# Kernel optimization log

Hardware: AMD Instinct MI355X
Metric: run time of the kernel (lower is better)

## Reference

```python
import jax, jax.numpy as jnp
import numpy as np

B, S, D_IN, D_EMB = 8, 2048, 512, 512

def setup_inputs() -> dict:
    key = jax.random.key(0)
    ks = jax.random.split(key, 7)
    s = 1.0 / np.sqrt(D_IN)
    return {
        "x": jax.random.normal(ks[0], (B, S, D_IN), dtype=jnp.float32),
        "Wq": jax.random.uniform(ks[1], (D_IN, D_EMB), jnp.float32, -s, s),
        "bq": jax.random.uniform(ks[2], (D_EMB,), jnp.float32, -s, s),
        "Wk": jax.random.uniform(ks[3], (D_IN, D_EMB), jnp.float32, -s, s),
        "bk": jax.random.uniform(ks[4], (D_EMB,), jnp.float32, -s, s),
        "Wv": jax.random.uniform(ks[5], (D_IN, D_EMB), jnp.float32, -s, s),
        "bv": jax.random.uniform(ks[6], (D_EMB,), jnp.float32, -s, s),
    }

def reference(x, Wq, bq, Wk, bk, Wv, bv):
    # single-head attention: softmax(QK^T / sqrt(d)) V
    q = x @ Wq + bq            # [B,S,E]
    k = x @ Wk + bk
    v = x @ Wv + bv
    scores = jnp.einsum('bse,bte->bst', q, k) / jnp.sqrt(jnp.float32(D_EMB))
    attn = jax.nn.softmax(scores, axis=-1)  # [B,S,S]
    return jnp.einsum('bst,bte->bse', attn, v)
```

## Files before the change

kernel.cpp:

```cpp
#include <hip/hip_runtime.h>
#include <stdint.h>


using f32x4 = __attribute__((ext_vector_type(4))) float;
using s16x8 = __attribute__((ext_vector_type(8))) short;
using u16x4 = __attribute__((ext_vector_type(4))) unsigned short;

#define S_LEN 2048
#define EMB   512

#define ASYNC16(g, l)                                                     \
  __builtin_amdgcn_global_load_lds(                                       \
      (const __attribute__((address_space(1))) void*)(g),                 \
      (__attribute__((address_space(3))) void*)(l), 16, 0, 0)

__device__ __forceinline__ unsigned short f2bf(float f) {
  union { float f; unsigned u; } v; v.f = f;
  unsigned r = v.u + 0x7fffu + ((v.u >> 16) & 1u);
  return (unsigned short)(r >> 16);
}

__global__ __launch_bounds__(256) void xconv_kernel(
    const float* __restrict__ x, short* __restrict__ xb) {
  int i = (blockIdx.x * 256 + threadIdx.x) * 8;
  f32x4 a = *(const f32x4*)(x + i);
  f32x4 b = *(const f32x4*)(x + i + 4);
  s16x8 h;
  h[0] = (short)f2bf(a[0]); h[1] = (short)f2bf(a[1]);
  h[2] = (short)f2bf(a[2]); h[3] = (short)f2bf(a[3]);
  h[4] = (short)f2bf(b[0]); h[5] = (short)f2bf(b[1]);
  h[6] = (short)f2bf(b[2]); h[7] = (short)f2bf(b[3]);
  *(s16x8*)(xb + i) = h;
}

__global__ __launch_bounds__(256) void wconv_kernel(
    const float* __restrict__ Wq, const float* __restrict__ Wk,
    const float* __restrict__ Wv, short* __restrict__ Wt) {
  int idx = blockIdx.x * 256 + threadIdx.x;
  int mat = idx >> 18;
  int r   = idx & 262143;
  int n   = r >> 9;
  int k   = r & 511;
  const float* W = (mat == 0) ? Wq : (mat == 1) ? Wk : Wv;
  Wt[idx] = (short)f2bf(W[k * 512 + n]);
}

__global__ __launch_bounds__(256) void qkv_gemm(
    const short* __restrict__ xb, const short* __restrict__ Wt,
    const float* __restrict__ bq, const float* __restrict__ bk,
    const float* __restrict__ bv,
    short* __restrict__ Qg, short* __restrict__ Kg, short* __restrict__ VTg) {
  __shared__ __align__(16) short As[128 * 64];
  __shared__ __align__(16) short Bs[128 * 64];
  int gid = blockIdx.x;
  int mat = gid >> 9;
  int rem = gid & 511;
  int mt  = rem & 127, nt = rem >> 7;
  int m0  = mt << 7,   n0 = nt << 7;
  const short* W    = Wt + (size_t)mat * 262144;
  const float* bias = (mat == 0) ? bq : (mat == 1) ? bk : bv;

  int tid = threadIdx.x, lane = tid & 63, wv = tid >> 6;
  int l16 = lane & 15, quad = lane >> 4;
  int wr = (wv & 1) << 6, wc = (wv >> 1) << 6;
  int drow = lane >> 3;
  int dchk = (lane & 7) ^ drow;

  const f32x4 Z4 = {0.f, 0.f, 0.f, 0.f};
  f32x4 acc[4][4];
#pragma unroll
  for (int a = 0; a < 4; ++a)
#pragma unroll
    for (int c = 0; c < 4; ++c) acc[a][c] = Z4;

  for (int it = 0; it < 8; ++it) {
    int k0 = it << 6;
    __syncthreads();
#pragma unroll
    for (int i = 0; i < 4; ++i) {
      int g   = wv * 4 + i;
      int row = g * 8 + drow;
      ASYNC16(xb + (size_t)(m0 + row) * 512 + k0 + dchk * 8, &As[g * 512]);
    }
#pragma unroll
    for (int i = 0; i < 4; ++i) {
      int g   = wv * 4 + i;
      int row = g * 8 + drow;
      ASYNC16(W + (size_t)(n0 + row) * 512 + k0 + dchk * 8, &Bs[g * 512]);
    }
    __syncthreads();
#pragma unroll
    for (int kk = 0; kk < 2; ++kk) {
      s16x8 af[4], bfr[4];
#pragma unroll
      for (int rb = 0; rb < 4; ++rb) {
        int row = wr + rb * 16 + l16;
        int c   = kk * 4 + quad;
        af[rb] = *(const s16x8*)(As + row * 64 + ((c ^ (row & 7)) * 8));
      }
#pragma unroll
      for (int cb = 0; cb < 4; ++cb) {
        int row = wc + cb * 16 + l16;
        int c   = kk * 4 + quad;
        bfr[cb] = *(const s16x8*)(Bs + row * 64 + ((c ^ (row & 7)) * 8));
      }
#pragma unroll
      for (int rb = 0; rb < 4; ++rb)
#pragma unroll
        for (int cb = 0; cb < 4; ++cb)
          acc[rb][cb] = __builtin_amdgcn_mfma_f32_16x16x32_bf16(af[rb], bfr[cb], acc[rb][cb], 0, 0, 0);
    }
  }

  float bsv[4];
#pragma unroll
  for (int cb = 0; cb < 4; ++cb) bsv[cb] = bias[n0 + wc + cb * 16 + l16];

  if (mat < 2) {
    short* D = (mat == 0) ? Qg : Kg;
#pragma unroll
    for (int rb = 0; rb < 4; ++rb)
#pragma unroll
      for (int cb = 0; cb < 4; ++cb)
#pragma unroll
        for (int r = 0; r < 4; ++r) {
          int m = m0 + wr + rb * 16 + quad * 4 + r;
          D[(size_t)m * 512 + n0 + wc + cb * 16 + l16] =
              (short)f2bf(acc[rb][cb][r] + bsv[cb]);
        }
  } else {
#pragma unroll
    for (int rb = 0; rb < 4; ++rb)
#pragma unroll
      for (int cb = 0; cb < 4; ++cb) {
        u16x4 h;
#pragma unroll
        for (int r = 0; r < 4; ++r) h[r] = f2bf(acc[rb][cb][r] + bsv[cb]);
        int m  = m0 + wr + rb * 16 + quad * 4;
        int bb = m >> 11, s = m & 2047;
        int e  = n0 + wc + cb * 16 + l16;
        *(u16x4*)(VTg + ((size_t)bb * 512 + e) * 2048 + s) = h;
      }
  }
}

__global__ __launch_bounds__(256, 2) void attn_kernel(
    const short* __restrict__ Qg, const short* __restrict__ Kg,
    const short* __restrict__ VTg, float* __restrict__ out) {
  __shared__ __align__(16) short Kt[32 * 512];
  __shared__ __align__(16) short Vt[512 * 32];
  __shared__ __align__(16) short Pl[32 * 48];
  __shared__ float l_l[32];
  const float SCL2 = 0.06375871855f;

  int b = blockIdx.x & 7, qt = blockIdx.x >> 3;
  int s0 = qt << 5;
  int tid = threadIdx.x, lane = tid & 63, wv = tid >> 6;
  int l16 = lane & 15, quad = lane >> 4;
  int a = wv & 1, h = wv >> 1;
  int e0 = wv << 7;

  const short* Kb = Kg  + ((size_t)b * S_LEN) * 512;
  const short* Vb = VTg + ((size_t)b * 512) * 2048;

  const short* kdma[8];
#pragma unroll
  for (int i = 0; i < 8; ++i) {
    int r = wv * 8 + i;
    kdma[i] = Kb + (size_t)r * 512 + ((lane ^ (i & 7)) * 8);
  }
  int v_er = lane >> 2;
  const short* vdma[8];
#pragma unroll
  for (int i = 0; i < 8; ++i) {
    int g = wv * 8 + i;
    int e = g * 16 + v_er;
    int vc = (lane & 3) ^ ((e >> 1) & 3);
    vdma[i] = Vb + (size_t)e * 2048 + vc * 8;
  }

#pragma unroll
  for (int i = 0; i < 8; ++i)
    ASYNC16(kdma[i], &Kt[(wv * 8 + i) * 512]);

  const short* qrow = Qg + ((size_t)b * S_LEN + s0 + a * 16 + l16) * 512 + quad * 8;
  s16x8 qf[16];
#pragma unroll
  for (int kk = 0; kk < 16; ++kk) qf[kk] = *(const s16x8*)(qrow + kk * 32);

  const f32x4 Z4 = {0.f, 0.f, 0.f, 0.f};
  f32x4 acc[2][8];
#pragma unroll
  for (int rb = 0; rb < 2; ++rb)
#pragma unroll
    for (int cb = 0; cb < 8; ++cb) acc[rb][cb] = Z4;
  f32x4 lsum = Z4;

  __syncthreads();

  for (int kt = 0; kt < 64; ++kt) {
    int t0 = kt << 5;
#pragma unroll
    for (int i = 0; i < 8; ++i)
      ASYNC16(vdma[i] + t0, &Vt[(wv * 8 + i) * 512]);

    f32x4 s_a = Z4, s_b = Z4;
    int krow = h * 16 + l16;
    const short* kb = &Kt[krow * 512];
    int ksw = (krow & 7);
#pragma unroll
    for (int kk = 0; kk < 8; ++kk) {
      s16x8 kf0 = *(const s16x8*)(kb + (((2 * kk) * 4 + quad) ^ ksw) * 8);
      s_a = __builtin_amdgcn_mfma_f32_16x16x32_bf16(qf[2 * kk], kf0, s_a, 0, 0, 0);
      s16x8 kf1 = *(const s16x8*)(kb + (((2 * kk + 1) * 4 + quad) ^ ksw) * 8);
      s_b = __builtin_amdgcn_mfma_f32_16x16x32_bf16(qf[2 * kk + 1], kf1, s_b, 0, 0, 0);
    }
    f32x4 sv = s_a + s_b;

    unsigned short pb[4];
#pragma unroll
    for (int r = 0; r < 4; ++r) {
      float p = exp2f(sv[r] * SCL2);
      pb[r] = f2bf(p);
      lsum[r] += p;
    }
#pragma unroll
    for (int r = 0; r < 4; ++r)
      Pl[(a * 16 + quad * 4 + r) * 48 + h * 16 + l16] = (short)pb[r];

    __syncthreads();

    if (kt + 1 < 64) {
      size_t adv = (size_t)(kt + 1) * 32 * 512;
#pragma unroll
      for (int i = 0; i < 8; ++i)
        ASYNC16(kdma[i] + adv, &Kt[(wv * 8 + i) * 512]);
    }

    s16x8 pf[2];
#pragma unroll
    for (int rb = 0; rb < 2; ++rb)
      pf[rb] = *(const s16x8*)(Pl + (rb * 16 + l16) * 48 + quad * 8);
#pragma unroll
    for (int cb = 0; cb < 8; ++cb) {
      int e  = e0 + cb * 16 + l16;
      int pc = quad ^ ((e >> 1) & 3);
      s16x8 vf = *(const s16x8*)(Vt + e * 32 + pc * 8);
#pragma unroll
      for (int rb = 0; rb < 2; ++rb)
        acc[rb][cb] = __builtin_amdgcn_mfma_f32_16x16x32_bf16(pf[rb], vf, acc[rb][cb], 0, 0, 0);
    }

    __syncthreads();
  }

#pragma unroll
  for (int r = 0; r < 4; ++r) {
    float v = lsum[r];
    v += __shfl_xor(v, 1);
    v += __shfl_xor(v, 2);
    v += __shfl_xor(v, 4);
    v += __shfl_xor(v, 8);
    lsum[r] = v;
  }
  if (h == 0 && l16 == 0) {
#pragma unroll
    for (int r = 0; r < 4; ++r) l_l[a * 16 + quad * 4 + r] = lsum[r];
  }
  __syncthreads();
  if (h == 1 && l16 == 0) {
#pragma unroll
    for (int r = 0; r < 4; ++r) l_l[a * 16 + quad * 4 + r] += lsum[r];
  }
  __syncthreads();

#pragma unroll
  for (int rb = 0; rb < 2; ++rb) {
    f32x4 lv = *(const f32x4*)(l_l + rb * 16 + quad * 4);
    f32x4 li;
#pragma unroll
    for (int r = 0; r < 4; ++r) li[r] = 1.0f / lv[r];
#pragma unroll
    for (int cb = 0; cb < 8; ++cb)
#pragma unroll
      for (int r = 0; r < 4; ++r)
        out[((size_t)b * S_LEN + s0 + rb * 16 + quad * 4 + r) * 512 + e0 + cb * 16 + l16] =
            acc[rb][cb][r] * li[r];
  }
}

extern "C" void kernel_launch(void* const* d_in, const int* in_sizes, int n_in,
                              void* d_out, int out_size, void* d_ws, size_t ws_size,
                              hipStream_t stream) {
  const float* x  = (const float*)d_in[0];
  const float* Wq = (const float*)d_in[1];
  const float* bq = (const float*)d_in[2];
  const float* Wk = (const float*)d_in[3];
  const float* bk = (const float*)d_in[4];
  const float* Wv = (const float*)d_in[5];
  const float* bv = (const float*)d_in[6];

  short* Wt  = (short*)d_ws;
  short* xb  = (short*)((char*)d_ws + 1572864);
  short* Qg  = xb + (size_t)8388608;
  short* Kg  = Qg + (size_t)8388608;
  short* VTg = Kg + (size_t)8388608;

  xconv_kernel<<<4096, 256, 0, stream>>>(x, xb);
  wconv_kernel<<<3072, 256, 0, stream>>>(Wq, Wk, Wv, Wt);
  qkv_gemm<<<1536, 256, 0, stream>>>(xb, Wt, bq, bk, bv, Qg, Kg, VTg);
  attn_kernel<<<512, 256, 0, stream>>>(Qg, Kg, VTg, (float*)d_out);
}
```

Before: 258.9 us.

## Widen attention key tile to 64, read V from global, share K fragments

The attention loop now handles 64 keys per iteration instead of 32, halving the iteration count and the number of block barriers. Each wave owns 16 keys and computes scores for both 16-row query halves, so one K fragment load from LDS feeds two MFMAs. The V shared-memory tile is removed and V fragments are loaded straight from global memory (L2) inside the PV stage. The trade-offs are a larger K tile in LDS, more registers for two sets of Q fragments, and exposed global-load latency on V with no prefetch, which may hurt occupancy or stall the MFMA pipeline.

```diff
diff --git a/kernel.cpp b/kernel.cpp
--- a/kernel.cpp
+++ b/kernel.cpp
@@ -147,146 +147,134 @@
 __global__ __launch_bounds__(256, 2) void attn_kernel(
     const short* __restrict__ Qg, const short* __restrict__ Kg,
     const short* __restrict__ VTg, float* __restrict__ out) {
-  __shared__ __align__(16) short Kt[32 * 512];
-  __shared__ __align__(16) short Vt[512 * 32];
-  __shared__ __align__(16) short Pl[32 * 48];
-  __shared__ float l_l[32];
+  __shared__ __align__(16) short Kt[64 * 512];
+  __shared__ __align__(16) short Pl[32 * 72];
+  __shared__ float Ls[4][32];
   const float SCL2 = 0.06375871855f;
 
   int b = blockIdx.x & 7, qt = blockIdx.x >> 3;
   int s0 = qt << 5;
   int tid = threadIdx.x, lane = tid & 63, wv = tid >> 6;
   int l16 = lane & 15, quad = lane >> 4;
-  int a = wv & 1, h = wv >> 1;
+  int kq = wv;
   int e0 = wv << 7;
 
   const short* Kb = Kg  + ((size_t)b * S_LEN) * 512;
   const short* Vb = VTg + ((size_t)b * 512) * 2048;
 
-  const short* kdma[8];
-#pragma unroll
-  for (int i = 0; i < 8; ++i) {
-    int r = wv * 8 + i;
-    kdma[i] = Kb + (size_t)r * 512 + ((lane ^ (i & 7)) * 8);
-  }
-  int v_er = lane >> 2;
-  const short* vdma[8];
-#pragma unroll
-  for (int i = 0; i < 8; ++i) {
-    int g = wv * 8 + i;
-    int e = g * 16 + v_er;
-    int vc = (lane & 3) ^ ((e >> 1) & 3);
-    vdma[i] = Vb + (size_t)e * 2048 + vc * 8;
-  }
-
-#pragma unroll
-  for (int i = 0; i < 8; ++i)
-    ASYNC16(kdma[i], &Kt[(wv * 8 + i) * 512]);
-
-  const short* qrow = Qg + ((size_t)b * S_LEN + s0 + a * 16 + l16) * 512 + quad * 8;
-  s16x8 qf[16];
-#pragma unroll
-  for (int kk = 0; kk < 16; ++kk) qf[kk] = *(const s16x8*)(qrow + kk * 32);
+#pragma unroll
+  for (int i = 0; i < 16; ++i) {
+    int r = wv * 16 + i;
+    ASYNC16(Kb + (size_t)r * 512 + ((lane ^ (i & 7)) * 8), &Kt[r * 512]);
+  }
+
+  s16x8 qf[2][16];
+#pragma unroll
+  for (int a = 0; a < 2; ++a) {
+    const short* qrow = Qg + ((size_t)b * S_LEN + s0 + a * 16 + l16) * 512 + quad * 8;
+#pragma unroll
+    for (int kk = 0; kk < 16; ++kk) qf[a][kk] = *(const s16x8*)(qrow + kk * 32);
+  }
 
   const f32x4 Z4 = {0.f, 0.f, 0.f, 0.f};
   f32x4 acc[2][8];
 #pragma unroll
-  for (int rb = 0; rb < 2; ++rb)
-#pragma unroll
-    for (int cb = 0; cb < 8; ++cb) acc[rb][cb] = Z4;
-  f32x4 lsum = Z4;
+  for (int a = 0; a < 2; ++a)
+#pragma unroll
+    for (int cb = 0; cb < 8; ++cb) acc[a][cb] = Z4;
+  f32x4 lsum[2] = {Z4, Z4};
+
+  const short* vrow = Vb + (size_t)(e0 + l16) * 2048 + quad * 8;
 
   __syncthreads();
 
-  for (int kt = 0; kt < 64; ++kt) {
-    int t0 = kt << 5;
-#pragma unroll
-    for (int i = 0; i < 8; ++i)
-      ASYNC16(vdma[i] + t0, &Vt[(wv * 8 + i) * 512]);
-
+  for (int kt = 0; kt < 32; ++kt) {
+    int krow = kq * 16 + l16;
+    const short* kb = &Kt[krow * 512];
+    int ksw = krow & 7;
     f32x4 s_a = Z4, s_b = Z4;
-    int krow = h * 16 + l16;
-    const short* kb = &Kt[krow * 512];
-    int ksw = (krow & 7);
-#pragma unroll
-    for (int kk = 0; kk < 8; ++kk) {
-      s16x8 kf0 = *(const s16x8*)(kb + (((2 * kk) * 4 + quad) ^ ksw) * 8);
-      s_a = __builtin_amdgcn_mfma_f32_16x16x32_bf16(qf[2 * kk], kf0, s_a, 0, 0, 0);
-      s16x8 kf1 = *(const s16x8*)(kb + (((2 * kk + 1) * 4 + quad) ^ ksw) * 8);
-      s_b = __builtin_amdgcn_mfma_f32_16x16x32_bf16(qf[2 * kk + 1], kf1, s_b, 0, 0, 0);
-    }
-    f32x4 sv = s_a + s_b;
-
-    unsigned short pb[4];
+#pragma unroll
+    for (int kk = 0; kk < 16; ++kk) {
+      s16x8 kf = *(const s16x8*)(kb + ((kk * 4 + quad) ^ ksw) * 8);
+      s_a = __builtin_amdgcn_mfma_f32_16x16x32_bf16(qf[0][kk], kf, s_a, 0, 0, 0);
+      s_b = __builtin_amdgcn_mfma_f32_16x16x32_bf16(qf[1][kk], kf, s_b, 0, 0, 0);
+    }
+
 #pragma unroll
     for (int r = 0; r < 4; ++r) {
-      float p = exp2f(sv[r] * SCL2);
-      pb[r] = f2bf(p);
-      lsum[r] += p;
-    }
-#pragma unroll
-    for (int r = 0; r < 4; ++r)
-      Pl[(a * 16 + quad * 4 + r) * 48 + h * 16 + l16] = (short)pb[r];
+      float p0 = exp2f(s_a[r] * SCL2);
+      float p1 = exp2f(s_b[r] * SCL2);
+      lsum[0][r] += p0;
+      lsum[1][r] += p1;
+      Pl[(quad * 4 + r) * 72 + kq * 16 + l16]        = (short)f2bf(p0);
+      Pl[(16 + quad * 4 + r) * 72 + kq * 16 + l16]   = (short)f2bf(p1);
+    }
 
     __syncthreads();
 
-    if (kt + 1 < 64) {
-      size_t adv = (size_t)(kt + 1) * 32 * 512;
-#pragma unroll
-      for (int i = 0; i < 8; ++i)
-        ASYNC16(kdma[i] + adv, &Kt[(wv * 8 + i) * 512]);
-    }
-
-    s16x8 pf[2];
-#pragma unroll
-    for (int rb = 0; rb < 2; ++rb)
-      pf[rb] = *(const s16x8*)(Pl + (rb * 16 + l16) * 48 + quad * 8);
-#pragma unroll
-    for (int cb = 0; cb < 8; ++cb) {
-      int e  = e0 + cb * 16 + l16;
-      int pc = quad ^ ((e >> 1) & 3);
-      s16x8 vf = *(const s16x8*)(Vt + e * 32 + pc * 8);
-#pragma unroll
-      for (int rb = 0; rb < 2; ++rb)
-        acc[rb][cb] = __builtin_amdgcn_mfma_f32_16x16x32_bf16(pf[rb], vf, acc[rb][cb], 0, 0, 0);
+    if (kt + 1 < 32) {
+      size_t adv = (size_t)(kt + 1) * 64 * 512;
+#pragma unroll
+      for (int i = 0; i < 16; ++i) {
+        int r = wv * 16 + i;
+        ASYNC16(Kb + adv + (size_t)r * 512 + ((lane ^ (i & 7)) * 8), &Kt[r * 512]);
+      }
+    }
+
+    const short* vt = vrow + kt * 64;
+#pragma unroll
+    for (int kc = 0; kc < 2; ++kc) {
+      s16x8 pf0 = *(const s16x8*)(Pl + l16 * 72 + kc * 32 + quad * 8);
+      s16x8 pf1 = *(const s16x8*)(Pl + (16 + l16) * 72 + kc * 32 + quad * 8);
+      s16x8 vf[8];
+#pragma unroll
+      for (int cb = 0; cb < 8; ++cb)
+        vf[cb] = *(const s16x8*)(vt + (size_t)cb * 32768 + kc * 32);
+#pragma unroll
+      for (int cb = 0; cb < 8; ++cb) {
+        acc[0][cb] = __builtin_amdgcn_mfma_f32_16x16x32_bf16(pf0, vf[cb], acc[0][cb], 0, 0, 0);
+        acc[1][cb] = __builtin_amdgcn_mfma_f32_16x16x32_bf16(pf1, vf[cb], acc[1][cb], 0, 0, 0);
+      }
     }
 
     __syncthreads();
   }
 
 #pragma unroll
-  for (int r = 0; r < 4; ++r) {
-    float v = lsum[r];
-    v += __shfl_xor(v, 1);
-    v += __shfl_xor(v, 2);
-    v += __shfl_xor(v, 4);
-    v += __shfl_xor(v, 8);
-    lsum[r] = v;
-  }
-  if (h == 0 && l16 == 0) {
-#pragma unroll
-    for (int r = 0; r < 4; ++r) l_l[a * 16 + quad * 4 + r] = lsum[r];
+  for (int a = 0; a < 2; ++a)
+#pragma unroll
+    for (int r = 0; r < 4; ++r) {
+      float v = lsum[a][r];
+      v += __shfl_xor(v, 1);
+      v += __shfl_xor(v, 2);
+      v += __shfl_xor(v, 4);
+      v += __shfl_xor(v, 8);
+      lsum[a][r] = v;
+    }
+  if (l16 == 0) {
+#pragma unroll
+    for (int a = 0; a < 2; ++a)
+#pragma unroll
+      for (int r = 0; r < 4; ++r) Ls[wv][a * 16 + quad * 4 + r] = lsum[a][r];
   }
   __syncthreads();
-  if (h == 1 && l16 == 0) {
-#pragma unroll
-    for (int r = 0; r < 4; ++r) l_l[a * 16 + quad * 4 + r] += lsum[r];
-  }
-  __syncthreads();
-
-#pragma unroll
-  for (int rb = 0; rb < 2; ++rb) {
-    f32x4 lv = *(const f32x4*)(l_l + rb * 16 + quad * 4);
-    f32x4 li;
-#pragma unroll
-    for (int r = 0; r < 4; ++r) li[r] = 1.0f / lv[r];
+
+  float linv[2][4];
+#pragma unroll
+  for (int a = 0; a < 2; ++a)
+#pragma unroll
+    for (int r = 0; r < 4; ++r) {
+      int srow = a * 16 + quad * 4 + r;
+      linv[a][r] = 1.0f / (Ls[0][srow] + Ls[1][srow] + Ls[2][srow] + Ls[3][srow]);
+    }
+#pragma unroll
+  for (int a = 0; a < 2; ++a)
 #pragma unroll
     for (int cb = 0; cb < 8; ++cb)
 #pragma unroll
       for (int r = 0; r < 4; ++r)
-        out[((size_t)b * S_LEN + s0 + rb * 16 + quad * 4 + r) * 512 + e0 + cb * 16 + l16] =
-            acc[rb][cb][r] * li[r];
-  }
+        out[((size_t)b * S_LEN + s0 + a * 16 + quad * 4 + r) * 512 + e0 + cb * 16 + l16] =
+            acc[a][cb][r] * linv[a][r];
 }
 
 extern "C" void kernel_launch(void* const* d_in, const int* in_sizes, int n_in,
```

Result: slower. 380.7 us (+47.1%).

## Load V fragments directly from global and merge conversion kernels

Applied to the files above, without the earlier changes.

The attention kernel stops staging V tiles in LDS through async copies. Each wave now loads its own V fragments straight from global memory into registers, which cuts the Vt buffer and shrinks the P scratch padding, reducing LDS use and potentially raising occupancy. The two fp32-to-bf16 conversion kernels are merged into one launch to save launch overhead. The cost is more register pressure (eight extra vector fragments per thread) and global-load latency sitting in the loop with no LDS-level sharing.

```diff
diff --git a/kernel.cpp b/kernel.cpp
--- a/kernel.cpp
+++ b/kernel.cpp
@@ -20,29 +20,30 @@
   return (unsigned short)(r >> 16);
 }
 
-__global__ __launch_bounds__(256) void xconv_kernel(
-    const float* __restrict__ x, short* __restrict__ xb) {
-  int i = (blockIdx.x * 256 + threadIdx.x) * 8;
-  f32x4 a = *(const f32x4*)(x + i);
-  f32x4 b = *(const f32x4*)(x + i + 4);
-  s16x8 h;
-  h[0] = (short)f2bf(a[0]); h[1] = (short)f2bf(a[1]);
-  h[2] = (short)f2bf(a[2]); h[3] = (short)f2bf(a[3]);
-  h[4] = (short)f2bf(b[0]); h[5] = (short)f2bf(b[1]);
-  h[6] = (short)f2bf(b[2]); h[7] = (short)f2bf(b[3]);
-  *(s16x8*)(xb + i) = h;
-}
-
-__global__ __launch_bounds__(256) void wconv_kernel(
-    const float* __restrict__ Wq, const float* __restrict__ Wk,
-    const float* __restrict__ Wv, short* __restrict__ Wt) {
-  int idx = blockIdx.x * 256 + threadIdx.x;
-  int mat = idx >> 18;
-  int r   = idx & 262143;
-  int n   = r >> 9;
-  int k   = r & 511;
-  const float* W = (mat == 0) ? Wq : (mat == 1) ? Wk : Wv;
-  Wt[idx] = (short)f2bf(W[k * 512 + n]);
+__global__ __launch_bounds__(256) void conv_kernel(
+    const float* __restrict__ x, const float* __restrict__ Wq,
+    const float* __restrict__ Wk, const float* __restrict__ Wv,
+    short* __restrict__ xb, short* __restrict__ Wt) {
+  int bid = blockIdx.x;
+  if (bid < 4096) {
+    int i = (bid * 256 + threadIdx.x) * 8;
+    f32x4 a = *(const f32x4*)(x + i);
+    f32x4 b = *(const f32x4*)(x + i + 4);
+    s16x8 h;
+    h[0] = (short)f2bf(a[0]); h[1] = (short)f2bf(a[1]);
+    h[2] = (short)f2bf(a[2]); h[3] = (short)f2bf(a[3]);
+    h[4] = (short)f2bf(b[0]); h[5] = (short)f2bf(b[1]);
+    h[6] = (short)f2bf(b[2]); h[7] = (short)f2bf(b[3]);
+    *(s16x8*)(xb + i) = h;
+  } else {
+    int idx = (bid - 4096) * 256 + threadIdx.x;
+    int mat = idx >> 18;
+    int r   = idx & 262143;
+    int n   = r >> 9;
+    int k   = r & 511;
+    const float* W = (mat == 0) ? Wq : (mat == 1) ? Wk : Wv;
+    Wt[idx] = (short)f2bf(W[k * 512 + n]);
+  }
 }
 
 __global__ __launch_bounds__(256) void qkv_gemm(
@@ -148,8 +149,7 @@
     const short* __restrict__ Qg, const short* __restrict__ Kg,
     const short* __restrict__ VTg, float* __restrict__ out) {
   __shared__ __align__(16) short Kt[32 * 512];
-  __shared__ __align__(16) short Vt[512 * 32];
-  __shared__ __align__(16) short Pl[32 * 48];
+  __shared__ __align__(16) short Pl[32 * 40];
   __shared__ float l_l[32];
   const float SCL2 = 0.06375871855f;
 
@@ -165,19 +165,8 @@
 
   const short* kdma[8];
 #pragma unroll
-  for (int i = 0; i < 8; ++i) {
-    int r = wv * 8 + i;
-    kdma[i] = Kb + (size_t)r * 512 + ((lane ^ (i & 7)) * 8);
-  }
-  int v_er = lane >> 2;
-  const short* vdma[8];
-#pragma unroll
-  for (int i = 0; i < 8; ++i) {
-    int g = wv * 8 + i;
-    int e = g * 16 + v_er;
-    int vc = (lane & 3) ^ ((e >> 1) & 3);
-    vdma[i] = Vb + (size_t)e * 2048 + vc * 8;
-  }
+  for (int i = 0; i < 8; ++i)
+    kdma[i] = Kb + (size_t)(wv * 8 + i) * 512 + ((lane ^ i) * 8);
 
 #pragma unroll
   for (int i = 0; i < 8; ++i)
@@ -196,18 +185,20 @@
     for (int cb = 0; cb < 8; ++cb) acc[rb][cb] = Z4;
   f32x4 lsum = Z4;
 
+  const short* vrow = Vb + (size_t)(e0 + l16) * 2048 + quad * 8;
+
   __syncthreads();
 
   for (int kt = 0; kt < 64; ++kt) {
-    int t0 = kt << 5;
-#pragma unroll
-    for (int i = 0; i < 8; ++i)
-      ASYNC16(vdma[i] + t0, &Vt[(wv * 8 + i) * 512]);
+    s16x8 vf[8];
+#pragma unroll
+    for (int cb = 0; cb < 8; ++cb)
+      vf[cb] = *(const s16x8*)(vrow + (size_t)cb * 32768 + kt * 32);
 
     f32x4 s_a = Z4, s_b = Z4;
     int krow = h * 16 + l16;
     const short* kb = &Kt[krow * 512];
-    int ksw = (krow & 7);
+    int ksw = krow & 7;
 #pragma unroll
     for (int kk = 0; kk < 8; ++kk) {
       s16x8 kf0 = *(const s16x8*)(kb + (((2 * kk) * 4 + quad) ^ ksw) * 8);
@@ -217,16 +208,12 @@
     }
     f32x4 sv = s_a + s_b;
 
-    unsigned short pb[4];
 #pragma unroll
     for (int r = 0; r < 4; ++r) {
       float p = exp2f(sv[r] * SCL2);
-      pb[r] = f2bf(p);
       lsum[r] += p;
-    }
-#pragma unroll
-    for (int r = 0; r < 4; ++r)
-      Pl[(a * 16 + quad * 4 + r) * 48 + h * 16 + l16] = (short)pb[r];
+      Pl[(a * 16 + quad * 4 + r) * 40 + h * 16 + l16] = (short)f2bf(p);
+    }
 
     __syncthreads();
 
@@ -240,15 +227,12 @@
     s16x8 pf[2];
 #pragma unroll
     for (int rb = 0; rb < 2; ++rb)
-      pf[rb] = *(const s16x8*)(Pl + (rb * 16 + l16) * 48 + quad * 8);
+      pf[rb] = *(const s16x8*)(Pl + (rb * 16 + l16) * 40 + quad * 8);
 #pragma unroll
     for (int cb = 0; cb < 8; ++cb) {
-      int e  = e0 + cb * 16 + l16;
-      int pc = quad ^ ((e >> 1) & 3);
-      s16x8 vf = *(const s16x8*)(Vt + e * 32 + pc * 8);
 #pragma unroll
       for (int rb = 0; rb < 2; ++rb)
-        acc[rb][cb] = __builtin_amdgcn_mfma_f32_16x16x32_bf16(pf[rb], vf, acc[rb][cb], 0, 0, 0);
+        acc[rb][cb] = __builtin_amdgcn_mfma_f32_16x16x32_bf16(pf[rb], vf[cb], acc[rb][cb], 0, 0, 0);
     }
 
     __syncthreads();
@@ -306,8 +290,7 @@
   short* Kg  = Qg + (size_t)8388608;
   short* VTg = Kg + (size_t)8388608;
 
-  xconv_kernel<<<4096, 256, 0, stream>>>(x, xb);
-  wconv_kernel<<<3072, 256, 0, stream>>>(Wq, Wk, Wv, Wt);
+  conv_kernel<<<7168, 256, 0, stream>>>(x, Wq, Wk, Wv, xb, Wt);
   qkv_gemm<<<1536, 256, 0, stream>>>(xb, Wt, bq, bk, bv, Qg, Kg, VTg);
   attn_kernel<<<512, 256, 0, stream>>>(Qg, Kg, VTg, (float*)d_out);
 }
```

Measured after the change: 290.1 us. 12.0% more time.

## Merge conversion kernels and stage V-transpose stores through shared memory

Applied to the files above, without the earlier changes.

Fuses the x and weight bf16 conversion kernels into a single launch, dropping one kernel launch. The V projection epilogue now writes its tile to a padded shared buffer and then emits coalesced 16-byte stores along the sequence axis, replacing scattered 8-byte transposed writes. Shared memory in the GEMM grows to hold the staging tile, which may cut occupancy. The softmax P-store loop is also merged, a cosmetic change.

```diff
diff --git a/kernel.cpp b/kernel.cpp
--- a/kernel.cpp
+++ b/kernel.cpp
@@ -20,29 +20,30 @@
   return (unsigned short)(r >> 16);
 }
 
-__global__ __launch_bounds__(256) void xconv_kernel(
-    const float* __restrict__ x, short* __restrict__ xb) {
-  int i = (blockIdx.x * 256 + threadIdx.x) * 8;
-  f32x4 a = *(const f32x4*)(x + i);
-  f32x4 b = *(const f32x4*)(x + i + 4);
-  s16x8 h;
-  h[0] = (short)f2bf(a[0]); h[1] = (short)f2bf(a[1]);
-  h[2] = (short)f2bf(a[2]); h[3] = (short)f2bf(a[3]);
-  h[4] = (short)f2bf(b[0]); h[5] = (short)f2bf(b[1]);
-  h[6] = (short)f2bf(b[2]); h[7] = (short)f2bf(b[3]);
-  *(s16x8*)(xb + i) = h;
-}
-
-__global__ __launch_bounds__(256) void wconv_kernel(
-    const float* __restrict__ Wq, const float* __restrict__ Wk,
-    const float* __restrict__ Wv, short* __restrict__ Wt) {
-  int idx = blockIdx.x * 256 + threadIdx.x;
-  int mat = idx >> 18;
-  int r   = idx & 262143;
-  int n   = r >> 9;
-  int k   = r & 511;
-  const float* W = (mat == 0) ? Wq : (mat == 1) ? Wk : Wv;
-  Wt[idx] = (short)f2bf(W[k * 512 + n]);
+__global__ __launch_bounds__(256) void conv_kernel(
+    const float* __restrict__ x, const float* __restrict__ Wq,
+    const float* __restrict__ Wk, const float* __restrict__ Wv,
+    short* __restrict__ xb, short* __restrict__ Wt) {
+  int bid = blockIdx.x;
+  if (bid < 4096) {
+    int i = (bid * 256 + threadIdx.x) * 8;
+    f32x4 a = *(const f32x4*)(x + i);
+    f32x4 b = *(const f32x4*)(x + i + 4);
+    s16x8 h;
+    h[0] = (short)f2bf(a[0]); h[1] = (short)f2bf(a[1]);
+    h[2] = (short)f2bf(a[2]); h[3] = (short)f2bf(a[3]);
+    h[4] = (short)f2bf(b[0]); h[5] = (short)f2bf(b[1]);
+    h[6] = (short)f2bf(b[2]); h[7] = (short)f2bf(b[3]);
+    *(s16x8*)(xb + i) = h;
+  } else {
+    int idx = (bid - 4096) * 256 + threadIdx.x;
+    int mat = idx >> 18;
+    int r   = idx & 262143;
+    int n   = r >> 9;
+    int k   = r & 511;
+    const float* W = (mat == 0) ? Wq : (mat == 1) ? Wk : Wv;
+    Wt[idx] = (short)f2bf(W[k * 512 + n]);
+  }
 }
 
 __global__ __launch_bounds__(256) void qkv_gemm(
@@ -50,8 +51,9 @@
     const float* __restrict__ bq, const float* __restrict__ bk,
     const float* __restrict__ bv,
     short* __restrict__ Qg, short* __restrict__ Kg, short* __restrict__ VTg) {
-  __shared__ __align__(16) short As[128 * 64];
-  __shared__ __align__(16) short Bs[128 * 64];
+  __shared__ __align__(16) short smem[128 * 132];
+  short* As = smem;
+  short* Bs = smem + 8192;
   int gid = blockIdx.x;
   int mat = gid >> 9;
   int rem = gid & 511;
@@ -129,18 +131,30 @@
               (short)f2bf(acc[rb][cb][r] + bsv[cb]);
         }
   } else {
+    __syncthreads();
 #pragma unroll
     for (int rb = 0; rb < 4; ++rb)
 #pragma unroll
       for (int cb = 0; cb < 4; ++cb) {
-        u16x4 h;
-#pragma unroll
-        for (int r = 0; r < 4; ++r) h[r] = f2bf(acc[rb][cb][r] + bsv[cb]);
-        int m  = m0 + wr + rb * 16 + quad * 4;
-        int bb = m >> 11, s = m & 2047;
-        int e  = n0 + wc + cb * 16 + l16;
-        *(u16x4*)(VTg + ((size_t)bb * 512 + e) * 2048 + s) = h;
+        int ln = wc + cb * 16 + l16;
+#pragma unroll
+        for (int r = 0; r < 4; ++r) {
+          int lm = wr + rb * 16 + quad * 4 + r;
+          smem[lm * 132 + ln] = (short)f2bf(acc[rb][cb][r] + bsv[cb]);
+        }
       }
+    __syncthreads();
+    int bb = m0 >> 11, sloc = m0 & 2047;
+    int c  = tid & 15;
+    int eb = (tid >> 4) * 8;
+#pragma unroll
+    for (int i = 0; i < 8; ++i) {
+      int e = eb + i;
+      s16x8 h;
+#pragma unroll
+      for (int j = 0; j < 8; ++j) h[j] = smem[(c * 8 + j) * 132 + e];
+      *(s16x8*)(VTg + ((size_t)bb * 512 + n0 + e) * 2048 + sloc + c * 8) = h;
+    }
   }
 }
 
@@ -217,16 +231,12 @@
     }
     f32x4 sv = s_a + s_b;
 
-    unsigned short pb[4];
 #pragma unroll
     for (int r = 0; r < 4; ++r) {
       float p = exp2f(sv[r] * SCL2);
-      pb[r] = f2bf(p);
       lsum[r] += p;
-    }
-#pragma unroll
-    for (int r = 0; r < 4; ++r)
-      Pl[(a * 16 + quad * 4 + r) * 48 + h * 16 + l16] = (short)pb[r];
+      Pl[(a * 16 + quad * 4 + r) * 48 + h * 16 + l16] = (short)f2bf(p);
+    }
 
     __syncthreads();
 
@@ -306,8 +316,7 @@
   short* Kg  = Qg + (size_t)8388608;
   short* VTg = Kg + (size_t)8388608;
 
-  xconv_kernel<<<4096, 256, 0, stream>>>(x, xb);
-  wconv_kernel<<<3072, 256, 0, stream>>>(Wq, Wk, Wv, Wt);
+  conv_kernel<<<7168, 256, 0, stream>>>(x, Wq, Wk, Wv, xb, Wt);
   qkv_gemm<<<1536, 256, 0, stream>>>(xb, Wt, bq, bk, bv, Qg, Kg, VTg);
   attn_kernel<<<512, 256, 0, stream>>>(Qg, Kg, VTg, (float*)d_out);
 }
```

After: 284.1 us. 1.1x slower.
